# Kernel tuning notes

Measured on AMD Instinct MI355X. Metric: run time of the kernel, lower is better.

## Reference

```python
import jax, jax.numpy as jnp
import numpy as np

B, S, HID, OP, NVAR = 4096, 1024, 30, 30, 4
# norm table passed as [[0,1],...,[0,1]] -> norm[0]=(0,1), norm[4]=(0,1)
N00, N01, N40, N41 = 0.0, 1.0, 0.0, 1.0


def setup_inputs() -> dict:
    key = jax.random.key(0)
    k = jax.random.split(key, 12)
    f32 = jnp.float32
    return {
        "x": jax.random.normal(k[0], (B, S, 4), f32),
        "var": jax.random.normal(k[1], (B, NVAR), f32),
        "amps": jax.random.uniform(k[2], (B, 2), f32, 0.5, 1.5),
        "s0": jnp.zeros((B, OP), f32),
        "W_dnn1": jax.random.normal(k[3], (1, OP + NVAR), f32) * 0.1,
        "b_dnn1": jnp.zeros((1,), f32),
        "W_x2h": jax.random.normal(k[4], (HID, 7), f32) * 0.2,
        "W_h2h": jax.random.normal(k[5], (HID, HID), f32) * 0.1,
        "W_dnn2": jax.random.normal(k[6], (1, HID), f32) * 0.1 + 0.2,
        "b_dnn2": jnp.zeros((1,), f32),
        "W_m1": jax.random.normal(k[7], (64, NVAR + 1), f32) * 0.1,
        "b_m1": jnp.zeros((64,), f32),
        "W_m2": jax.random.normal(k[8], (32, 64), f32) * 0.1,
        "b_m2": jnp.zeros((32,), f32),
        "W_m3": jax.random.normal(k[9], (1, 32), f32) * 0.1,
        "b_m3": jnp.zeros((1,), f32),
        "n_init": 16,
    }


def reference(x, var, amps, s0, W_dnn1, b_dnn1, W_x2h, W_h2h, W_dnn2, b_dnn2,
              W_m1, b_m1, W_m2, b_m2, W_m3, b_m3, n_init):
    dt = x.dtype
    # stop-operator thresholds: linspace(5/OP, 5, OP), shape (1, OP)
    r = jnp.linspace(5.0 / OP, 5.0, OP, dtype=dt).reshape(1, OP)
    x2 = jnp.concatenate([x[:, :, 0:1], x[:, :, 2:4]], axis=2)  # (B,S,3)
    dB = x[:, :, 1:2]  # (B,S,1)

    def hyst(s):  # dnn1 over concat(stop-operator state, var)
        return jnp.concatenate([s, var], axis=1) @ W_dnn1.T + b_dnn1  # (B,1)

    # --- t = 0 (special init of the eddy hidden state) ---
    s1 = jnp.clip((dB[:, 0] + s0) / r, -1.0, 1.0) * r  # (B,OP)
    H_hyst0 = hyst(s1)
    H_eddy_init = x[:, 0, 0:1] - H_hyst0  # (B,1)
    h2 = jnp.ones((x.shape[0], HID), dt) / jnp.sum(W_dnn2, axis=1) * H_eddy_init
    h2 = jax.nn.sigmoid(jnp.concatenate([x2[:, 0], var], axis=1) @ W_x2h.T + h2 @ W_h2h.T)
    H0 = H_hyst0 + h2 @ W_dnn2.T + b_dnn2  # (B,1)

    # --- t = 1..S-1 via scan ---
    def step(carry, xs):
        s1, h2 = carry
        dB_t, x2_t = xs  # (B,1), (B,3)
        s1 = jnp.clip((dB_t + s1) / r, -1.0, 1.0) * r
        H_hyst = hyst(s1)
        h2 = jax.nn.sigmoid(jnp.concatenate([x2_t, var], axis=1) @ W_x2h.T + h2 @ W_h2h.T)
        return (s1, h2), H_hyst + h2 @ W_dnn2.T + b_dnn2

    xs = (jnp.swapaxes(dB[:, 1:], 0, 1), jnp.swapaxes(x2[:, 1:], 0, 1))
    _, Hs = jax.lax.scan(step, (s1, h2), xs)  # (S-1,B,1)
    output = jnp.concatenate([H0[:, None, :], jnp.swapaxes(Hs, 0, 1)], axis=1)  # (B,S,1)

    H = output[:, n_init:, :]
    B_amp = x[:, n_init:, 0:1] * amps[:, 0:1][:, None, :]
    H_amp = H * amps[:, 1:2][:, None, :]
    # trapezoid rule along time axis with non-uniform x spacing
    dxb = B_amp[:, 1:] - B_amp[:, :-1]
    P_prelim = jnp.sum(dxb * (H_amp[:, 1:] + H_amp[:, :-1]) * 0.5, axis=1)  # (B,1)
    P_prelim = P_prelim * 10.0 ** (var[:, 0:1] * N01 + N00)
    Pcv = (jnp.log10(jnp.clip(P_prelim, 1e-12)) - N40) / N41

    # loss MLP (eval mode: dropout = identity)
    mlp_in = jnp.concatenate([var, Pcv], axis=1)  # (B,5)
    h = jax.nn.relu(mlp_in @ W_m1.T + b_m1)
    h = jax.nn.relu(h @ W_m2.T + b_m2)
    s = h @ W_m3.T + b_m3
    return H, Pcv + s
```

## Files before the change

### kernel.cpp

```cpp
#include <hip/hip_runtime.h>

#define B_TOT 4096
#define S_LEN 1024
#define HID 30
#define SKIP 16
#define HLEN (S_LEN - SKIP)
#define WARM 32

typedef float f32x4 __attribute__((ext_vector_type(4)));
typedef short bf16x8 __attribute__((ext_vector_type(8)));
typedef int   i32x4  __attribute__((ext_vector_type(4)));
typedef unsigned int u32x2 __attribute__((ext_vector_type(2)));

template <int CTRL>
__device__ __forceinline__ float dppmov(float v) {
  return __int_as_float(__builtin_amdgcn_update_dpp(
      0, __float_as_int(v), CTRL, 0xF, 0xF, true));
}
template <int CTRL>
__device__ __forceinline__ float dpp_add(float v) { return v + dppmov<CTRL>(v); }
__device__ __forceinline__ float red16(float v) {
  v = dpp_add<0xB1>(v); v = dpp_add<0x4E>(v);
  v = dpp_add<0x141>(v); v = dpp_add<0x140>(v);
  return v;
}
__device__ __forceinline__ float sigmoid_fast(float z) {
  float e = __builtin_amdgcn_exp2f(z * -1.442695041f);
  return __builtin_amdgcn_rcpf(1.0f + e);
}
__device__ __forceinline__ int cvt_pk_bf16(float a, float b) {
  int r; asm("v_cvt_pk_bf16_f32 %0, %1, %2" : "=v"(r) : "v"(a), "v"(b)); return r;
}
__device__ __forceinline__ void split8(const float* v, int* hw, int* lw) {
#pragma unroll
  for (int p = 0; p < 4; ++p) {
    int h = cvt_pk_bf16(v[2*p], v[2*p+1]);
    float f0 = __int_as_float(h << 16);
    float f1 = __int_as_float(h & 0xffff0000);
    lw[p] = cvt_pk_bf16(v[2*p] - f0, v[2*p+1] - f1);
    hw[p] = h;
  }
}
__device__ __forceinline__ bf16x8 frag4(const int* w) {
  return __builtin_bit_cast(bf16x8, (i32x4){w[0], w[1], w[2], w[3]});
}

__device__ __forceinline__ float redq(float v) {
#if __has_builtin(__builtin_amdgcn_permlane16_swap) && __has_builtin(__builtin_amdgcn_permlane32_swap)
  unsigned iv = __float_as_uint(v);
  u32x2 p = __builtin_amdgcn_permlane16_swap(iv, iv, false, false);
  float s = __uint_as_float(p[0]) + __uint_as_float(p[1]);
  unsigned is = __float_as_uint(s);
  u32x2 qq = __builtin_amdgcn_permlane32_swap(is, is, false, false);
  return __uint_as_float(qq[0]) + __uint_as_float(qq[1]);
#else
  v += __int_as_float(__builtin_amdgcn_ds_swizzle(__float_as_int(v), 0x401F));
  int l = (int)(threadIdx.x & 63);
  v += __int_as_float(__builtin_amdgcn_ds_bpermute(((l ^ 32) << 2),
                                                   __float_as_int(v)));
  return v;
#endif
}

__global__ __launch_bounds__(256) void mminet_fused(
    const float* __restrict__ x,   const float* __restrict__ var,
    const float* __restrict__ amps,const float* __restrict__ s0,
    const float* __restrict__ W1,  const float* __restrict__ b1,
    const float* __restrict__ Wx,  const float* __restrict__ Wh,
    const float* __restrict__ W2,  const float* __restrict__ b2,
    const float* __restrict__ Wm1, const float* __restrict__ bm1,
    const float* __restrict__ Wm2, const float* __restrict__ bm2,
    const float* __restrict__ Wm3, const float* __restrict__ bm3,
    float* __restrict__ Hout, float* __restrict__ out2)
{
  __shared__ float Pred[4][16];
  __shared__ float mlpbuf[16][64];

  const int tid   = threadIdx.x;
  const int l     = tid & 63;
  const int chunk = tid >> 6;
  const int q     = l >> 4;
  const int c     = l & 15;
  const int b     = blockIdx.x * 16 + c;

  const int ob = (chunk == 0) ? SKIP : (chunk == 1) ? 280 : (chunk == 2) ? 528 : 776;
  const int oe = (chunk == 0) ? 280  : (chunk == 1) ? 528 : (chunk == 2) ? 776 : 1024;
  const int ps = (chunk == 0) ? SKIP : ((ob - WARM) & ~31);

  const float v0 = var[b*4+0], v1 = var[b*4+1], v2 = var[b*4+2], v3 = var[b*4+3];

  float wx0[8], wx1[8], wx2[8], cva[8], w1a[8], w2a[8], rc[8], s1[8];
#pragma unroll
  for (int i = 0; i < 8; ++i) {
    const int row = (i < 4) ? (4*q + i) : (16 + 4*q + (i - 4));
    if (row < HID) {
      wx0[i] = Wx[row*7+0]; wx1[i] = Wx[row*7+1]; wx2[i] = Wx[row*7+2];
      cva[i] = Wx[row*7+3]*v0 + Wx[row*7+4]*v1 + Wx[row*7+5]*v2 + Wx[row*7+6]*v3;
      w1a[i] = W1[row]; w2a[i] = W2[row];
      rc[i]  = 5.0f * (float)(row + 1) / 30.0f;
      s1[i]  = s0[b*HID + row];
    } else {
      wx0[i]=wx1[i]=wx2[i]=cva[i]=w1a[i]=w2a[i]=s1[i]=0.f; rc[i]=1.0f;
    }
  }

  float a1v[8], a2v[8];
#pragma unroll
  for (int kk = 0; kk < 8; ++kk) {
    const int u = (kk < 4) ? (4*q + kk) : (16 + 4*q + (kk - 4));
    a1v[kk] = (u < HID) ? Wh[c*HID + u] : 0.f;
    a2v[kk] = (u < HID && (16 + c) < HID) ? Wh[(16+c)*HID + u] : 0.f;
  }
  int t0[4], t1[4], t2[4], t3[4];
  split8(a1v, t0, t1); split8(a2v, t2, t3);
  const bf16x8 A1h = frag4(t0), A1l = frag4(t1);
  const bf16x8 A2h = frag4(t2), A2l = frag4(t3);

  const float hcst = W1[30]*v0 + W1[31]*v1 + W1[32]*v2 + W1[33]*v3 + b1[0];
  const float hc2  = hcst + b2[0];

  float sw = 0.f;
#pragma unroll
  for (int i = 0; i < 8; ++i) sw += w2a[i];
  const float sumW2 = redq(sw);

  const float4* xb = (const float4*)(x + (size_t)b * S_LEN * 4);

  bf16x8 Bhi, Blo;
  auto packB = [&](const float* hv) {
    int bh[4], bl[4];
    split8(hv, bh, bl);
    Bhi = frag4(bh); Blo = frag4(bl);
  };

  auto dostep = [&](const float4 xq) -> float {
#pragma unroll
    for (int i = 0; i < 8; ++i)
      s1[i] = __builtin_amdgcn_fmed3f(s1[i] + xq.y, -rc[i], rc[i]);
    f32x4 zi0, zi1;
#pragma unroll
    for (int i = 0; i < 4; ++i) {
      zi0[i] = cva[i]   + wx0[i]*xq.x   + wx1[i]*xq.z   + wx2[i]*xq.w;
      zi1[i] = cva[i+4] + wx0[i+4]*xq.x + wx1[i+4]*xq.z + wx2[i+4]*xq.w;
    }
    const f32x4 zz = {0.f, 0.f, 0.f, 0.f};
    f32x4 a0 = __builtin_amdgcn_mfma_f32_16x16x32_bf16(A1h, Bhi, zi0, 0, 0, 0);
    f32x4 b0 = __builtin_amdgcn_mfma_f32_16x16x32_bf16(A1l, Bhi, zz,  0, 0, 0);
    f32x4 c0 = __builtin_amdgcn_mfma_f32_16x16x32_bf16(A1h, Blo, zz,  0, 0, 0);
    f32x4 a1 = __builtin_amdgcn_mfma_f32_16x16x32_bf16(A2h, Bhi, zi1, 0, 0, 0);
    f32x4 b1v= __builtin_amdgcn_mfma_f32_16x16x32_bf16(A2l, Bhi, zz,  0, 0, 0);
    f32x4 c1 = __builtin_amdgcn_mfma_f32_16x16x32_bf16(A2h, Blo, zz,  0, 0, 0);
    f32x4 z0 = (a0 + b0) + c0;
    f32x4 z1 = (a1 + b1v) + c1;
    float hv[8];
#pragma unroll
    for (int i = 0; i < 4; ++i) {
      hv[i]     = sigmoid_fast(z0[i]);
      hv[4 + i] = sigmoid_fast(z1[i]);
    }
    packB(hv);
    float hp = 0.f;
#pragma unroll
    for (int i = 0; i < 8; ++i)
      hp = fmaf(w1a[i], s1[i], fmaf(w2a[i], hv[i], hp));
    return redq(hp);
  };

  if (chunk == 0) {
    float4 xv = xb[0];
#pragma unroll
    for (int i = 0; i < 8; ++i)
      s1[i] = __builtin_amdgcn_fmed3f(s1[i] + xv.y, -rc[i], rc[i]);
    float hh = 0.f;
#pragma unroll
    for (int i = 0; i < 8; ++i) hh = fmaf(w1a[i], s1[i], hh);
    const float Hh0  = redq(hh) + hcst;
    const float hpre = (xv.x - Hh0) / sumW2;
    float hv[8];
#pragma unroll
    for (int i = 0; i < 8; ++i) {
      const int row = (i < 4) ? (4*q + i) : (16 + 4*q + (i - 4));
      float rs = 0.f;
      if (row < HID)
        for (int u2 = 0; u2 < HID; ++u2) rs += Wh[row*HID + u2];
      float z = cva[i] + wx0[i]*xv.x + wx1[i]*xv.z + wx2[i]*xv.w + rs*hpre;
      hv[i] = sigmoid_fast(z);
    }
    packB(hv);
    for (int t = 1; t < SKIP; ++t) (void)dostep(xb[t]);
  } else {
    const float* xf = x + (size_t)b * S_LEN * 4;
    float dc[32], dn[32];
#pragma unroll
    for (int u = 0; u < 32; ++u) dc[u] = xf[u*4 + 1];
    for (int t = 0; t < ps; t += 32) {
      const bool more = (t + 32 < ps);
      if (more) {
#pragma unroll
        for (int u = 0; u < 32; ++u) dn[u] = xf[(t + 32 + u)*4 + 1];
      }
#pragma unroll
      for (int u = 0; u < 32; ++u) {
#pragma unroll
        for (int i = 0; i < 8; ++i)
          s1[i] = __builtin_amdgcn_fmed3f(s1[i] + dc[u], -rc[i], rc[i]);
      }
      if (more) {
#pragma unroll
        for (int u = 0; u < 32; ++u) dc[u] = dn[u];
      }
    }
    float hv[8];
#pragma unroll
    for (int i = 0; i < 8; ++i) hv[i] = 0.5f;
    packB(hv);
  }

  float P = 0.f, Hprev = 0.f, Bprev = 0.f;
  float4 xc0 = xb[ps+0], xc1 = xb[ps+1], xc2 = xb[ps+2], xc3 = xb[ps+3];

  for (int t = ps; t < oe; t += 4) {
    const int tn = (t + 4 < oe) ? (t + 4) : t;
    float4 xn0 = xb[tn+0], xn1 = xb[tn+1], xn2 = xb[tn+2], xn3 = xb[tn+3];

    float hq0, hq1, hq2, hq3;
    {
      float Ht = dostep(xc0) + hc2;
      if (t + 0 > SKIP && t + 0 >= ob) P += (xc0.x - Bprev) * (Ht + Hprev);
      Hprev = Ht; Bprev = xc0.x; hq0 = Ht;
    }
    {
      float Ht = dostep(xc1) + hc2;
      if (t + 1 > SKIP && t + 1 >= ob) P += (xc1.x - Bprev) * (Ht + Hprev);
      Hprev = Ht; Bprev = xc1.x; hq1 = Ht;
    }
    {
      float Ht = dostep(xc2) + hc2;
      if (t + 2 > SKIP && t + 2 >= ob) P += (xc2.x - Bprev) * (Ht + Hprev);
      Hprev = Ht; Bprev = xc2.x; hq2 = Ht;
    }
    {
      float Ht = dostep(xc3) + hc2;
      if (t + 3 > SKIP && t + 3 >= ob) P += (xc3.x - Bprev) * (Ht + Hprev);
      Hprev = Ht; Bprev = xc3.x; hq3 = Ht;
    }
    if (t >= ob && l < 16) {
      *(float4*)(Hout + (size_t)b * HLEN + (t - SKIP)) =
          make_float4(hq0, hq1, hq2, hq3);
    }
    xc0 = xn0; xc1 = xn1; xc2 = xn2; xc3 = xn3;
  }

  if (l < 16) Pred[chunk][c] = P;
  __syncthreads();

  const int li = tid & 15;
  const int g  = tid >> 4;
  const int be = blockIdx.x * 16 + g;
  const float Ptot = Pred[0][g] + Pred[1][g] + Pred[2][g] + Pred[3][g];
  const float e0 = var[be*4+0], e1 = var[be*4+1], e2 = var[be*4+2], e3 = var[be*4+3];
  const float am0 = amps[be*2+0], am1 = amps[be*2+1];

  float Pp = Ptot * 0.5f * am0 * am1;
  Pp *= __builtin_amdgcn_exp2f(e0 * 3.321928095f);
  Pp = fmaxf(Pp, 1e-12f);
  const float Pcv = __builtin_amdgcn_logf(Pp) * 0.30102999566f;

  float* hs = &mlpbuf[g][0];
#pragma unroll
  for (int qq = 0; qq < 4; ++qq) {
    const int n = li + 16 * qq;
    const float* wr = Wm1 + n * 5;
    float h1v = bm1[n] + wr[0]*e0 + wr[1]*e1 + wr[2]*e2 + wr[3]*e3 + wr[4]*Pcv;
    hs[n] = fmaxf(h1v, 0.f);
  }
  const int m0 = li, m1 = li + 16;
  const float4* h1v4 = (const float4*)hs;
  const float4* w2a4 = (const float4*)(Wm2 + m0 * 64);
  const float4* w2b4 = (const float4*)(Wm2 + m1 * 64);
  float zz0 = bm2[m0], zz1 = bm2[m1];
#pragma unroll
  for (int qq = 0; qq < 16; ++qq) {
    float4 hh = h1v4[qq];
    float4 wa = w2a4[qq], wb = w2b4[qq];
    zz0 += wa.x*hh.x + wa.y*hh.y + wa.z*hh.z + wa.w*hh.w;
    zz1 += wb.x*hh.x + wb.y*hh.y + wb.z*hh.z + wb.w*hh.w;
  }
  float sp = Wm3[m0] * fmaxf(zz0, 0.f) + Wm3[m1] * fmaxf(zz1, 0.f);
  sp = red16(sp);
  if (li == 0) out2[be] = Pcv + sp + bm3[0];
}

extern "C" void kernel_launch(void* const* d_in, const int* in_sizes, int n_in,
                              void* d_out, int out_size, void* d_ws, size_t ws_size,
                              hipStream_t stream)
{
  const float* x    = (const float*)d_in[0];
  const float* var  = (const float*)d_in[1];
  const float* amps = (const float*)d_in[2];
  const float* s0   = (const float*)d_in[3];
  const float* W1   = (const float*)d_in[4];
  const float* b1   = (const float*)d_in[5];
  const float* Wx   = (const float*)d_in[6];
  const float* Wh   = (const float*)d_in[7];
  const float* W2   = (const float*)d_in[8];
  const float* b2   = (const float*)d_in[9];
  const float* Wm1  = (const float*)d_in[10];
  const float* bm1  = (const float*)d_in[11];
  const float* Wm2  = (const float*)d_in[12];
  const float* bm2  = (const float*)d_in[13];
  const float* Wm3  = (const float*)d_in[14];
  const float* bm3  = (const float*)d_in[15];

  float* Hout = (float*)d_out;
  float* out2 = (float*)d_out + (size_t)B_TOT * HLEN;

  mminet_fused<<<B_TOT / 16, 256, 0, stream>>>(
      x, var, amps, s0, W1, b1, Wx, Wh, W2, b2,
      Wm1, bm1, Wm2, bm2, Wm3, bm3, Hout, out2);
}
```

Baseline: 273.9 us.

## Split time chunks across two blocks and move loss MLP to separate kernel

The recurrent scan now splits each batch group's sequence into eight warm-started time chunks spread over two blocks instead of four chunks in one block, which doubles the grid and shortens each wave's serial chain. Partial trapezoid sums go to a workspace, and a second small kernel combines them and runs the loss MLP. This adds more warm-up recomputation per chunk, an extra launch, and a workspace round trip.

```diff
diff --git a/kernel.cpp b/kernel.cpp
--- a/kernel.cpp
+++ b/kernel.cpp
@@ -62,30 +62,33 @@
 #endif
 }
 
-__global__ __launch_bounds__(256) void mminet_fused(
+__global__ __launch_bounds__(256) void mminet_scan(
     const float* __restrict__ x,   const float* __restrict__ var,
-    const float* __restrict__ amps,const float* __restrict__ s0,
+    const float* __restrict__ s0,
     const float* __restrict__ W1,  const float* __restrict__ b1,
     const float* __restrict__ Wx,  const float* __restrict__ Wh,
     const float* __restrict__ W2,  const float* __restrict__ b2,
-    const float* __restrict__ Wm1, const float* __restrict__ bm1,
-    const float* __restrict__ Wm2, const float* __restrict__ bm2,
-    const float* __restrict__ Wm3, const float* __restrict__ bm3,
-    float* __restrict__ Hout, float* __restrict__ out2)
+    float* __restrict__ Hout, float* __restrict__ Pws)
 {
   __shared__ float Pred[4][16];
-  __shared__ float mlpbuf[16][64];
 
   const int tid   = threadIdx.x;
   const int l     = tid & 63;
-  const int chunk = tid >> 6;
+  const int cl    = tid >> 6;
+  const int half  = blockIdx.x & 1;
+  const int g     = blockIdx.x >> 1;
   const int q     = l >> 4;
   const int c     = l & 15;
-  const int b     = blockIdx.x * 16 + c;
-
-  const int ob = (chunk == 0) ? SKIP : (chunk == 1) ? 280 : (chunk == 2) ? 528 : 776;
-  const int oe = (chunk == 0) ? 280  : (chunk == 1) ? 528 : (chunk == 2) ? 776 : 1024;
-  const int ps = (chunk == 0) ? SKIP : ((ob - WARM) & ~31);
+  const int b     = g * 16 + c;
+
+  const int ob = (half == 0)
+      ? (cl == 0 ? 16  : cl == 1 ? 160 : cl == 2 ? 288 : 408)
+      : (cl == 0 ? 520 : cl == 1 ? 648 : cl == 2 ? 776 : 900);
+  const int oe = (half == 0)
+      ? (cl == 0 ? 160 : cl == 1 ? 288 : cl == 2 ? 408 : 520)
+      : (cl == 0 ? 648 : cl == 1 ? 776 : cl == 2 ? 900 : 1024);
+  const bool first = (half == 0) && (cl == 0);
+  const int ps = first ? SKIP : ((ob - WARM) & ~31);
 
   const float v0 = var[b*4+0], v1 = var[b*4+1], v2 = var[b*4+2], v3 = var[b*4+3];
 
@@ -166,7 +169,7 @@
     return redq(hp);
   };
 
-  if (chunk == 0) {
+  if (first) {
     float4 xv = xb[0];
 #pragma unroll
     for (int i = 0; i < 8; ++i)
@@ -251,13 +254,29 @@
     xc0 = xn0; xc1 = xn1; xc2 = xn2; xc3 = xn3;
   }
 
-  if (l < 16) Pred[chunk][c] = P;
+  if (l < 16) Pred[cl][c] = P;
   __syncthreads();
-
-  const int li = tid & 15;
-  const int g  = tid >> 4;
-  const int be = blockIdx.x * 16 + g;
-  const float Ptot = Pred[0][g] + Pred[1][g] + Pred[2][g] + Pred[3][g];
+  if (tid < 16) {
+    const int bb = g * 16 + tid;
+    Pws[bb * 2 + half] =
+        Pred[0][tid] + Pred[1][tid] + Pred[2][tid] + Pred[3][tid];
+  }
+}
+
+__global__ __launch_bounds__(256) void mminet_mlp(
+    const float* __restrict__ var, const float* __restrict__ amps,
+    const float* __restrict__ Wm1, const float* __restrict__ bm1,
+    const float* __restrict__ Wm2, const float* __restrict__ bm2,
+    const float* __restrict__ Wm3, const float* __restrict__ bm3,
+    const float* __restrict__ Pws, float* __restrict__ out2)
+{
+  __shared__ float mlpbuf[16][64];
+  const int tid = threadIdx.x;
+  const int li  = tid & 15;
+  const int g   = tid >> 4;
+  const int be  = blockIdx.x * 16 + g;
+
+  const float Ptot = Pws[be*2 + 0] + Pws[be*2 + 1];
   const float e0 = var[be*4+0], e1 = var[be*4+1], e2 = var[be*4+2], e3 = var[be*4+3];
   const float am0 = amps[be*2+0], am1 = amps[be*2+1];
 
@@ -314,8 +333,10 @@
 
   float* Hout = (float*)d_out;
   float* out2 = (float*)d_out + (size_t)B_TOT * HLEN;
-
-  mminet_fused<<<B_TOT / 16, 256, 0, stream>>>(
-      x, var, amps, s0, W1, b1, Wx, Wh, W2, b2,
-      Wm1, bm1, Wm2, bm2, Wm3, bm3, Hout, out2);
-}
+  float* Pws  = (float*)d_ws;
+
+  mminet_scan<<<(B_TOT / 16) * 2, 256, 0, stream>>>(
+      x, var, s0, W1, b1, Wx, Wh, W2, b2, Hout, Pws);
+  mminet_mlp<<<B_TOT / 16, 256, 0, stream>>>(
+      var, amps, Wm1, bm1, Wm2, bm2, Wm3, bm3, Pws, out2);
+}
```

Measured after the change: 397.1 us. 45.0% more time.
